# Performance work log

Measured on AMD Instinct MI355X. Metric: run time of the kernel, lower is better.

## Reference

```python
import jax, jax.numpy as jnp
import numpy as np

B, S, D = 2, 1024, 1024
H, HD = 16, 64          # n_heads, head_dim (H*HD == D)
E, FF = 8, 2816         # num_experts, moe hidden_dim
TOP_K = 2               # hard-coded torch.topk(scores, 2)
EPS = 1e-5


def rmsnorm(x, w):
    return x * jax.lax.rsqrt(jnp.mean(x * x, axis=-1, keepdims=True) + EPS) * w


def apply_rope(x, cos, sin):
    # x: [B,S,H,HD]; cos/sin: [S,HD//2] -> interleaved rotary (llama style)
    xr, xi = x[..., 0::2], x[..., 1::2]
    c = cos[None, :, None, :]
    s = sin[None, :, None, :]
    out_r = xr * c - xi * s
    out_i = xr * s + xi * c
    return jnp.stack([out_r, out_i], axis=-1).reshape(x.shape)


def setup_inputs() -> dict:
    key = jax.random.key(0)
    ks = jax.random.split(key, 10)
    sc = 0.02
    pos = jnp.arange(S, dtype=jnp.float32)
    inv = 1.0 / (10000.0 ** (jnp.arange(0, HD, 2, dtype=jnp.float32) / HD))
    ang = pos[:, None] * inv[None, :]                       # [S, HD//2]
    return {
        "x": jax.random.normal(ks[0], (B, S, D), jnp.float32),
        "freqs_cos": jnp.cos(ang),
        "freqs_sin": jnp.sin(ang),
        "attn_norm_w": jnp.ones((D,), jnp.float32),
        "wq": jax.random.normal(ks[1], (D, D), jnp.float32) * sc,
        "wk": jax.random.normal(ks[2], (D, D), jnp.float32) * sc,
        "wv": jax.random.normal(ks[3], (D, D), jnp.float32) * sc,
        "wo": jax.random.normal(ks[4], (D, D), jnp.float32) * sc,
        "ffn_norm_w": jnp.ones((D,), jnp.float32),
        "gate_w": jax.random.normal(ks[5], (E, D), jnp.float32) * sc,
        "w1": jax.random.normal(ks[6], (E, FF, D), jnp.float32) * sc,
        "w2": jax.random.normal(ks[7], (E, FF, D), jnp.float32) * sc,
        "w3": jax.random.normal(ks[8], (E, FF, D), jnp.float32) * sc,
    }


def reference(x, freqs_cos, freqs_sin, attn_norm_w, wq, wk, wv, wo,
              ffn_norm_w, gate_w, w1, w2, w3):
    b, s, d = x.shape

    # ---- pre-norm attention + residual ----
    xn = rmsnorm(x, attn_norm_w)
    q = (xn @ wq.T).reshape(b, s, H, HD)
    k = (xn @ wk.T).reshape(b, s, H, HD)
    v = (xn @ wv.T).reshape(b, s, H, HD)
    q = apply_rope(q, freqs_cos, freqs_sin)
    k = apply_rope(k, freqs_cos, freqs_sin)
    scores = jnp.einsum("bqhd,bkhd->bhqk", q, k) / jnp.sqrt(jnp.float32(HD))
    causal = jnp.tril(jnp.ones((s, s), bool))
    scores = jnp.where(causal[None, None], scores, jnp.finfo(scores.dtype).min)
    attn = jax.nn.softmax(scores, axis=-1)
    o = jnp.einsum("bhqk,bkhd->bqhd", attn, v).reshape(b, s, d) @ wo.T
    h = x + o

    # ---- top-2 MoE FFN (math identical to gather-per-token einsums) ----
    t = rmsnorm(h, ffn_norm_w).reshape(-1, d)               # [T, D]
    T = t.shape[0]
    gate = t @ gate_w.T                                     # [T, E]
    expert_weights, expert_idx = jax.lax.top_k(gate, TOP_K)
    expert_weights = jax.nn.softmax(expert_weights, axis=-1)  # [T, 2]

    x1 = jax.nn.silu(jnp.einsum("td,efd->tef", t, w1))      # [T, E, FF]
    x3 = jnp.einsum("td,efd->tef", t, w3)                   # [T, E, FF]
    ta = jnp.arange(T)[:, None]
    g = x1[ta, expert_idx] * x3[ta, expert_idx]             # [T, 2, FF]
    gw = g * expert_weights[..., None]                      # fold routing weights
    h_full = jnp.zeros((T, E, FF), t.dtype).at[ta, expert_idx].add(gw)
    moe = jnp.einsum("tef,efd->td", h_full, w2)             # [T, D]

    return h + moe.reshape(b, s, d)
```

## Files before the change

kernel.cpp:

```cpp
#include <hip/hip_runtime.h>

#define DI __device__ __forceinline__

typedef __attribute__((ext_vector_type(8))) short short8;
typedef __attribute__((ext_vector_type(4))) float f32x4;

#define DM   1024
#define TT   2048
#define SEQ  1024
#define NHD  16
#define HDD  64
#define NE   8
#define FF   2816

DI ushort f2bf(float f){
  union { float f; unsigned u; } c; c.f = f;
  unsigned u = c.u;
  u += 0x7fffu + ((u >> 16) & 1u);
  return (ushort)(u >> 16);
}
DI float bf2f(ushort b){
  union { unsigned u; float f; } c; c.u = ((unsigned)b) << 16;
  return c.f;
}
DI unsigned pk2(float a, float b){ return (unsigned)f2bf(a) | ((unsigned)f2bf(b) << 16); }
DI uint2 mku2(unsigned a, unsigned b){ uint2 r; r.x = a; r.y = b; return r; }

DI f32x4 MFMA(short8 a, short8 b, f32x4 c){
  return __builtin_amdgcn_mfma_f32_16x16x32_bf16(a, b, c, 0, 0, 0);
}

DI void gload16(const void* g, void* l){
  __builtin_amdgcn_global_load_lds(
      (const __attribute__((address_space(1))) unsigned*)g,
      (__attribute__((address_space(3))) unsigned*)l, 16, 0, 0);
}

#define LDSWZB(row, p) (((row) * 128) + ((((p) ^ ((row) & 7))) * 16))

__global__ __launch_bounds__(256) void k_pre(
    const float* __restrict__ x, const float* __restrict__ anw,
    ushort* __restrict__ xh, ushort* __restrict__ xl,
    const float* __restrict__ wq, const float* __restrict__ wk,
    const float* __restrict__ wv, const float* __restrict__ wo,
    ushort* __restrict__ wqh, ushort* __restrict__ wql,
    ushort* __restrict__ wkh, ushort* __restrict__ wkl,
    ushort* __restrict__ wvh, ushort* __restrict__ wvl,
    ushort* __restrict__ woh, ushort* __restrict__ wol)
{
  int bid = blockIdx.x, tid = threadIdx.x;
  if (bid >= 2048) {
    int q = bid - 2048;
    int y = q >> 10;
    const float* W = y == 0 ? wq : (y == 1 ? wk : (y == 2 ? wv : wo));
    ushort* H = y == 0 ? wqh : (y == 1 ? wkh : (y == 2 ? wvh : woh));
    ushort* L = y == 0 ? wql : (y == 1 ? wkl : (y == 2 ? wvl : wol));
    int i = (q & 1023) * 256 + tid;
    float4 v = ((const float4*)W)[i];
    ushort h0 = f2bf(v.x), h1 = f2bf(v.y), h2 = f2bf(v.z), h3 = f2bf(v.w);
    ((uint2*)H)[i] = mku2((unsigned)h0 | ((unsigned)h1 << 16),
                          (unsigned)h2 | ((unsigned)h3 << 16));
    ((uint2*)L)[i] = mku2(pk2(v.x - bf2f(h0), v.y - bf2f(h1)),
                          pk2(v.z - bf2f(h2), v.w - bf2f(h3)));
    return;
  }
  int row = bid;
  float4 v = ((const float4*)(x + (size_t)row * DM))[tid];
  float ss = v.x*v.x + v.y*v.y + v.z*v.z + v.w*v.w;
#pragma unroll
  for (int m = 32; m >= 1; m >>= 1) ss += __shfl_xor(ss, m);
  __shared__ float sh[4];
  if ((tid & 63) == 0) sh[tid >> 6] = ss;
  __syncthreads();
  ss = sh[0] + sh[1] + sh[2] + sh[3];
  float rstd = 1.0f / sqrtf(ss * (1.0f / DM) + 1e-5f);
  float4 wv2 = ((const float4*)anw)[tid];
  float o0 = v.x * rstd * wv2.x, o1 = v.y * rstd * wv2.y;
  float o2 = v.z * rstd * wv2.z, o3 = v.w * rstd * wv2.w;
  ushort h0 = f2bf(o0), h1 = f2bf(o1), h2 = f2bf(o2), h3 = f2bf(o3);
  ((uint2*)(xh + (size_t)row * DM))[tid] =
      mku2((unsigned)h0 | ((unsigned)h1 << 16), (unsigned)h2 | ((unsigned)h3 << 16));
  ((uint2*)(xl + (size_t)row * DM))[tid] =
      mku2(pk2(o0 - bf2f(h0), o1 - bf2f(h1)), pk2(o2 - bf2f(h2), o3 - bf2f(h3)));
}

__global__ __launch_bounds__(256) void k_cw13(const float* __restrict__ w1,
                                              const float* __restrict__ w3,
                                              ushort* __restrict__ w1b,
                                              ushort* __restrict__ w3b)
{
  const float* src = blockIdx.y ? w3 : w1;
  ushort* dst = blockIdx.y ? w3b : w1b;
  const size_t N4 = (size_t)NE * FF * DM / 4;
  for (size_t i = (size_t)blockIdx.x * 256 + threadIdx.x; i < N4;
       i += (size_t)gridDim.x * 256) {
    float4 v = ((const float4*)src)[i];
    ((uint2*)dst)[i] = mku2(pk2(v.x, v.y), pk2(v.z, v.w));
  }
}

__global__ __launch_bounds__(256, 3) void k_gemm_qkv(
    const ushort* __restrict__ xh, const ushort* __restrict__ xl,
    const ushort* __restrict__ wqh, const ushort* __restrict__ wql,
    const ushort* __restrict__ wkh, const ushort* __restrict__ wkl,
    const ushort* __restrict__ wvh, const ushort* __restrict__ wvl,
    const float* __restrict__ fc, const float* __restrict__ fs,
    ushort* __restrict__ qh, ushort* __restrict__ ql,
    ushort* __restrict__ kh, ushort* __restrict__ kl,
    ushort* __restrict__ vh, ushort* __restrict__ vl,
    const float* __restrict__ w2, ushort* __restrict__ w2t)
{
  __shared__ __align__(16) char lds[49152];
  int bid = blockIdx.x, tid = threadIdx.x;

  if (bid >= 768) {
    ushort* lt = (ushort*)lds;
    int pid = bid - 768;
    for (int tt = pid; tt < 16*44*8; tt += 512) {
      int dt = tt & 15, rest = tt >> 4;
      int ft = rest % 44, e = rest / 44;
#pragma unroll
      for (int i = 0; i < 4; i++) {
        int c = tid + i*256;
        int r = c >> 4, q = c & 15;
        float4 v = *(const float4*)(w2 + ((size_t)e*FF + ft*64 + r) * DM + dt*64 + q*4);
        lt[(q*4+0)*72 + r] = f2bf(v.x);
        lt[(q*4+1)*72 + r] = f2bf(v.y);
        lt[(q*4+2)*72 + r] = f2bf(v.z);
        lt[(q*4+3)*72 + r] = f2bf(v.w);
      }
      __syncthreads();
#pragma unroll
      for (int i = 0; i < 2; i++) {
        int c = tid + i*256;
        int d = c >> 3, fq = c & 7;
        *(uint4*)(w2t + ((size_t)e*DM + dt*64 + d) * FF + ft*64 + fq*8) =
            *(const uint4*)&lt[d*72 + fq*8];
      }
      __syncthreads();
    }
    return;
  }

  char* Ah = lds;          char* Al = lds + 16384;
  char* Bh = lds + 32768;  char* Bl = lds + 40960;
  int which = bid >> 8;
  int rest = bid & 255;
  int bnn = rest & 15, bm = rest >> 4;
  const ushort* WH = which == 0 ? wqh : (which == 1 ? wkh : wvh);
  const ushort* WL = which == 0 ? wql : (which == 1 ? wkl : wvl);
  int lane = tid & 63, w = tid >> 6;
  int r0 = lane >> 3, pp = lane & 7;
  size_t asrc[4]; int adst[4];
#pragma unroll
  for (int i = 0; i < 4; i++) {
    int c = w * 4 + i;
    int row = c * 8 + r0;
    asrc[i] = (size_t)(bm * 128 + row) * DM + (pp ^ r0) * 8;
    adst[i] = c * 1024;
  }
  size_t bsrc[2]; int bdst[2];
#pragma unroll
  for (int i = 0; i < 2; i++) {
    int c = 2 * w + i;
    int row = c * 8 + r0;
    bsrc[i] = (size_t)(bnn * 64 + row) * DM + (pp ^ r0) * 8;
    bdst[i] = c * 1024;
  }
  f32x4 acc[2][4] = {};
  for (int kb = 0; kb < DM; kb += 64) {
    __syncthreads();
#pragma unroll
    for (int i = 0; i < 4; i++) {
      gload16(xh + asrc[i] + kb, Ah + adst[i]);
      gload16(xl + asrc[i] + kb, Al + adst[i]);
    }
#pragma unroll
    for (int i = 0; i < 2; i++) {
      gload16(WH + bsrc[i] + kb, Bh + bdst[i]);
      gload16(WL + bsrc[i] + kb, Bl + bdst[i]);
    }
    __syncthreads();
#pragma unroll
    for (int kk = 0; kk < 2; kk++) {
      int j = kk * 4 + (lane >> 4);
      short8 ar[2], al[2];
#pragma unroll
      for (int mi = 0; mi < 2; mi++) {
        int row = w * 32 + mi * 16 + (lane & 15);
        ar[mi] = *(const short8*)(Ah + LDSWZB(row, j));
        al[mi] = *(const short8*)(Al + LDSWZB(row, j));
      }
#pragma unroll
      for (int ni = 0; ni < 4; ni++) {
        int n = ni * 16 + (lane & 15);
        short8 b_h = *(const short8*)(Bh + LDSWZB(n, j));
        short8 b_l = *(const short8*)(Bl + LDSWZB(n, j));
#pragma unroll
        for (int mi = 0; mi < 2; mi++) {
          acc[mi][ni] = MFMA(ar[mi], b_h, acc[mi][ni]);
          acc[mi][ni] = MFMA(al[mi], b_h, acc[mi][ni]);
          acc[mi][ni] = MFMA(ar[mi], b_l, acc[mi][ni]);
        }
      }
    }
  }
  ushort* OH = which == 0 ? qh : kh;
  ushort* OL = which == 0 ? ql : kl;
#pragma unroll
  for (int mi = 0; mi < 2; mi++)
#pragma unroll
    for (int ni = 0; ni < 4; ni++)
#pragma unroll
      for (int r = 0; r < 4; r++) {
        int rg = bm*128 + w*32 + mi*16 + (lane >> 4)*4 + r;
        int cg = bnn*64 + ni*16 + (lane & 15);
        float v = acc[mi][ni][r];
        int b = rg >> 10, s = rg & 1023, hh = cg >> 6, hd = cg & 63;
        if (which <= 1) {
          float p = __shfl_xor(v, 1);
          int pi = hd >> 1;
          float c = fc[s*32 + pi], sn = fs[s*32 + pi];
          float rr = (hd & 1) ? (p * sn + v * c) : (v * c - p * sn);
          size_t o = ((size_t)(b*NHD + hh) * SEQ + s) * HDD + hd;
          ushort hv = f2bf(rr);
          OH[o] = hv; OL[o] = f2bf(rr - bf2f(hv));
        } else {
          size_t o = ((size_t)((b*NHD + hh)*HDD + hd)) * SEQ + s;
          ushort hv = f2bf(v);
          vh[o] = hv; vl[o] = f2bf(v - bf2f(hv));
        }
      }
}

__global__ __launch_bounds__(256) void k_attn_prep(
    const ushort* __restrict__ qh_, const ushort* __restrict__ ql_,
    const ushort* __restrict__ kh_, const ushort* __restrict__ kl_,
    const ushort* __restrict__ vh_, const ushort* __restrict__ vl_,
    ushort* __restrict__ oh_, ushort* __restrict__ ol_,
    const float* __restrict__ w1, const float* __restrict__ w3,
    ushort* __restrict__ w1b, ushort* __restrict__ w3b)
{
  __shared__ __align__(16) char smem[49152];
  int bid = blockIdx.x, tid = threadIdx.x;

  if (bid >= 512) {
    int pid = bid - 512;
    const size_t N4 = (size_t)NE * FF * DM / 4;
    for (size_t i = (size_t)pid * 256 + tid; i < N4; i += (size_t)512 * 256) {
      float4 v = ((const float4*)w1)[i];
      ((uint2*)w1b)[i] = mku2(pk2(v.x, v.y), pk2(v.z, v.w));
      float4 u = ((const float4*)w3)[i];
      ((uint2*)w3b)[i] = mku2(pk2(u.x, u.y), pk2(u.z, u.w));
    }
    return;
  }

  char* Kh = smem;          char* Kl = smem + 8192;
  char* Vh = smem + 16384;  char* Vl = smem + 24576;
  ushort* Ph = (ushort*)(smem + 32768);
  ushort* Pl = (ushort*)(smem + 40960);
  int qt = bid & 15, bh = bid >> 4;
  int lane = tid & 63, w = tid >> 6;
  int r0 = lane >> 3, pp = lane & 7;
  short8 qfh[2], qfl[2];
  int qrow = qt*64 + w*16 + (lane & 15);
#pragma unroll
  for (int ks = 0; ks < 2; ks++) {
    size_t g = ((size_t)bh * SEQ + qrow) * HDD + ks*32 + (lane >> 4)*8;
    qfh[ks] = *(const short8*)(qh_ + g);
    qfl[ks] = *(const short8*)(ql_ + g);
  }
  size_t kbase[2], vbase[2];
#pragma unroll
  for (int i = 0; i < 2; i++) {
    int c = 2*w + i;
    kbase[i] = ((size_t)bh * SEQ + c*8 + r0) * 64 + (pp ^ r0) * 8;
    vbase[i] = ((size_t)bh * 64 + c*8 + r0) * SEQ + (pp ^ r0) * 8;
  }
  f32x4 oacc[4] = {};
  float mrun[4], lrun[4];
#pragma unroll
  for (int r = 0; r < 4; r++) { mrun[r] = -1e30f; lrun[r] = 0.0f; }

  for (int kt = 0; kt <= qt; kt++) {
    __syncthreads();
#pragma unroll
    for (int i = 0; i < 2; i++) {
      int c = 2*w + i;
      size_t ko = kbase[i] + (size_t)kt * 64 * 64;
      size_t vo = vbase[i] + (size_t)kt * 64;
      gload16(kh_ + ko, Kh + c*1024);
      gload16(kl_ + ko, Kl + c*1024);
      gload16(vh_ + vo, Vh + c*1024);
      gload16(vl_ + vo, Vl + c*1024);
    }
    __syncthreads();
    f32x4 sa[4] = {};
#pragma unroll
    for (int j2 = 0; j2 < 4; j2++) {
#pragma unroll
      for (int ks = 0; ks < 2; ks++) {
        int kr = j2*16 + (lane & 15);
        int j = ks*4 + (lane >> 4);
        short8 b_h = *(const short8*)(Kh + LDSWZB(kr, j));
        short8 b_l = *(const short8*)(Kl + LDSWZB(kr, j));
        sa[j2] = MFMA(qfh[ks], b_h, sa[j2]);
        sa[j2] = MFMA(qfl[ks], b_h, sa[j2]);
        sa[j2] = MFMA(qfh[ks], b_l, sa[j2]);
      }
    }
    float sv[4][4];
#pragma unroll
    for (int j2 = 0; j2 < 4; j2++)
#pragma unroll
      for (int r = 0; r < 4; r++) {
        float xx = sa[j2][r] * 0.125f;
        if (kt == qt) {
          int kv = j2*16 + (lane & 15), qi = w*16 + (lane >> 4)*4 + r;
          if (kv > qi) xx = -1e30f;
        }
        sv[j2][r] = xx;
      }
#pragma unroll
    for (int r = 0; r < 4; r++) {
      float mx = fmaxf(fmaxf(sv[0][r], sv[1][r]), fmaxf(sv[2][r], sv[3][r]));
#pragma unroll
      for (int m = 8; m >= 1; m >>= 1) mx = fmaxf(mx, __shfl_xor(mx, m));
      float mn = fmaxf(mrun[r], mx);
      float alp = __expf(mrun[r] - mn);
      mrun[r] = mn;
      float rs = 0.0f;
#pragma unroll
      for (int j2 = 0; j2 < 4; j2++) { float pv = __expf(sv[j2][r] - mn); sv[j2][r] = pv; rs += pv; }
#pragma unroll
      for (int m = 8; m >= 1; m >>= 1) rs += __shfl_xor(rs, m);
      lrun[r] = lrun[r] * alp + rs;
#pragma unroll
      for (int hf = 0; hf < 4; hf++) oacc[hf][r] *= alp;
    }
#pragma unroll
    for (int j2 = 0; j2 < 4; j2++)
#pragma unroll
      for (int r = 0; r < 4; r++) {
        int row = (lane >> 4)*4 + r, col = j2*16 + (lane & 15);
        int d = w*1024 + row*64 + (((col >> 3) ^ (row & 7)) * 8) + (col & 7);
        ushort hv = f2bf(sv[j2][r]);
        Ph[d] = hv; Pl[d] = f2bf(sv[j2][r] - bf2f(hv));
      }
#pragma unroll
    for (int hf = 0; hf < 4; hf++) {
#pragma unroll
      for (int ks = 0; ks < 2; ks++) {
        int prow = lane & 15;
        int j = ks*4 + (lane >> 4);
        int pg = (j ^ (prow & 7)) * 8;
        short8 pfh = *(const short8*)&Ph[w*1024 + prow*64 + pg];
        short8 pfl = *(const short8*)&Pl[w*1024 + prow*64 + pg];
        int vrow = hf*16 + (lane & 15);
        short8 vfh = *(const short8*)(Vh + LDSWZB(vrow, j));
        short8 vfl = *(const short8*)(Vl + LDSWZB(vrow, j));
        oacc[hf] = MFMA(pfh, vfh, oacc[hf]);
        oacc[hf] = MFMA(pfl, vfh, oacc[hf]);
        oacc[hf] = MFMA(pfh, vfl, oacc[hf]);
      }
    }
  }
  int b = bh >> 4, h = bh & 15;
#pragma unroll
  for (int r = 0; r < 4; r++) {
    float li = 1.0f / lrun[r];
    int srow = qt*64 + w*16 + (lane >> 4)*4 + r;
#pragma unroll
    for (int hf = 0; hf < 4; hf++) {
      float v = oacc[hf][r] * li;
      size_t o = ((size_t)(b*SEQ + srow)) * DM + h*HDD + hf*16 + (lane & 15);
      ushort hv = f2bf(v);
      oh_[o] = hv; ol_[o] = f2bf(v - bf2f(hv));
    }
  }
}

__global__ __launch_bounds__(256, 4) void k_gemm_wo(
    const ushort* __restrict__ oh, const ushort* __restrict__ ol,
    const ushort* __restrict__ woh, const ushort* __restrict__ wol,
    const float* __restrict__ x, float* __restrict__ hb)
{
  __shared__ __align__(16) char lds[32768];
  char* Ah = lds;          char* Al = lds + 8192;
  char* Bh = lds + 16384;  char* Bl = lds + 24576;
  int bnn = blockIdx.x, bm = blockIdx.y;
  int tid = threadIdx.x, lane = tid & 63, w = tid >> 6;
  int r0 = lane >> 3, pp = lane & 7;
  size_t asrc[2], bsrc[2]; int cdst[2];
#pragma unroll
  for (int i = 0; i < 2; i++) {
    int c = w * 2 + i;
    int row = c * 8 + r0;
    asrc[i] = (size_t)(bm * 64 + row) * DM + (pp ^ r0) * 8;
    bsrc[i] = (size_t)(bnn * 64 + row) * DM + (pp ^ r0) * 8;
    cdst[i] = c * 1024;
  }
  f32x4 acc[4] = {};
  for (int kb = 0; kb < DM; kb += 64) {
    __syncthreads();
#pragma unroll
    for (int i = 0; i < 2; i++) {
      gload16(oh + asrc[i] + kb, Ah + cdst[i]);
      gload16(ol + asrc[i] + kb, Al + cdst[i]);
      gload16(woh + bsrc[i] + kb, Bh + cdst[i]);
      gload16(wol + bsrc[i] + kb, Bl + cdst[i]);
    }
    __syncthreads();
#pragma unroll
    for (int kk = 0; kk < 2; kk++) {
      int j = kk * 4 + (lane >> 4);
      int row = w * 16 + (lane & 15);
      short8 ar = *(const short8*)(Ah + LDSWZB(row, j));
      short8 al = *(const short8*)(Al + LDSWZB(row, j));
#pragma unroll
      for (int ni = 0; ni < 4; ni++) {
        int n = ni * 16 + (lane & 15);
        short8 b_h = *(const short8*)(Bh + LDSWZB(n, j));
        short8 b_l = *(const short8*)(Bl + LDSWZB(n, j));
        acc[ni] = MFMA(ar, b_h, acc[ni]);
        acc[ni] = MFMA(al, b_h, acc[ni]);
        acc[ni] = MFMA(ar, b_l, acc[ni]);
      }
    }
  }
#pragma unroll
  for (int ni = 0; ni < 4; ni++)
#pragma unroll
    for (int r = 0; r < 4; r++) {
      int rg = bm*64 + w*16 + (lane >> 4)*4 + r;
      int cg = bnn*64 + ni*16 + (lane & 15);
      hb[(size_t)rg * DM + cg] = x[(size_t)rg * DM + cg] + acc[ni][r];
    }
}

__global__ __launch_bounds__(256) void k_gate(
    const float* __restrict__ hb, const float* __restrict__ fw, const float* __restrict__ gwt,
    ushort* __restrict__ tb, int* __restrict__ idx, float* __restrict__ ew,
    int* __restrict__ cnt, int* __restrict__ pos)
{
  int t = blockIdx.x, tid = threadIdx.x;
  float4 v = ((const float4*)(hb + (size_t)t * DM))[tid];
  float ss = v.x*v.x + v.y*v.y + v.z*v.z + v.w*v.w;
#pragma unroll
  for (int m = 32; m >= 1; m >>= 1) ss += __shfl_xor(ss, m);
  __shared__ float sh[4];
  if ((tid & 63) == 0) sh[tid >> 6] = ss;
  __syncthreads();
  ss = sh[0] + sh[1] + sh[2] + sh[3];
  float rstd = 1.0f / sqrtf(ss * (1.0f / DM) + 1e-5f);
  float4 wv = ((const float4*)fw)[tid];
  float tv0 = v.x*rstd*wv.x, tv1 = v.y*rstd*wv.y, tv2 = v.z*rstd*wv.z, tv3 = v.w*rstd*wv.w;
  ((uint2*)(tb + (size_t)t * DM))[tid] = mku2(pk2(tv0, tv1), pk2(tv2, tv3));
  float ge[8];
#pragma unroll
  for (int e = 0; e < 8; e++) {
    float4 gv = ((const float4*)(gwt + (size_t)e * DM))[tid];
    float s = tv0*gv.x + tv1*gv.y + tv2*gv.z + tv3*gv.w;
#pragma unroll
    for (int m = 32; m >= 1; m >>= 1) s += __shfl_xor(s, m);
    ge[e] = s;
  }
  __shared__ float gsh[4][8];
  if ((tid & 63) == 0) {
#pragma unroll
    for (int e = 0; e < 8; e++) gsh[tid >> 6][e] = ge[e];
  }
  __syncthreads();
  if (tid == 0) {
    float lg[8];
#pragma unroll
    for (int e = 0; e < 8; e++) lg[e] = gsh[0][e] + gsh[1][e] + gsh[2][e] + gsh[3][e];
    int i0 = 0;
    for (int e = 1; e < 8; e++) if (lg[e] > lg[i0]) i0 = e;
    int i1 = (i0 == 0) ? 1 : 0;
    for (int e = 0; e < 8; e++) if (e != i0 && lg[e] > lg[i1]) i1 = e;
    float ex = __expf(lg[i1] - lg[i0]);
    idx[2*t] = i0; idx[2*t+1] = i1;
    ew[2*t] = 1.0f / (1.0f + ex); ew[2*t+1] = ex / (1.0f + ex);
    pos[2*t]   = atomicAdd(&cnt[i0], 1);
    pos[2*t+1] = atomicAdd(&cnt[i1], 1);
  }
}

__global__ __launch_bounds__(256) void k_offscatter(
    const int* __restrict__ cnt, int* __restrict__ off, int* __restrict__ tmap,
    const int* __restrict__ idx, int* __restrict__ ent, int* __restrict__ pos)
{
  __shared__ int soff[8];
  int tid = threadIdx.x;
  if (tid == 0) {
    int a = 0, nt = 0;
    for (int e = 0; e < 8; e++) {
      off[e] = a; soff[e] = a; a += cnt[e];
      int m = (cnt[e] + 127) >> 7;
      for (int j = 0; j < m; j++) { tmap[1 + nt] = (e << 8) | j; nt++; }
    }
    tmap[0] = nt;
  }
  __syncthreads();
  for (int s = tid; s < 2*TT; s += 256) {
    int e = idx[s];
    int g = soff[e] + pos[s];
    ent[g] = s;
    pos[s] = g;
  }
}

__global__ __launch_bounds__(256, 4) void k_moe13(
    const ushort* __restrict__ tb, const ushort* __restrict__ w1b, const ushort* __restrict__ w3b,
    const int* __restrict__ ent, const float* __restrict__ ew,
    const int* __restrict__ cnt, const int* __restrict__ off, const int* __restrict__ tmap,
    ushort* __restrict__ gb)
{
  int y = blockIdx.y;
  if (y >= tmap[0]) return;
  int tm = tmap[1 + y];
  int e = tm >> 8, mt = tm & 255;
  int nt = blockIdx.x;
  int cn = cnt[e], oe = off[e];
  __shared__ __align__(16) char lds[32768];
  char* Ab = lds;
  char* B1 = lds + 16384;
  char* B3 = lds + 24576;
  int tid = threadIdx.x, lane = tid & 63, w = tid >> 6;
  int wr = w >> 1, wc = w & 1;
  int r0 = lane >> 3, pp = lane & 7;

  const ushort* abase = tb + (pp ^ r0) * 8;
  unsigned aoff[4];
#pragma unroll
  for (int i = 0; i < 4; i++) {
    int c = w * 4 + i;
    int r = c * 8 + r0;
    int g = oe + mt * 128 + r; if (g > 2*TT - 1) g = 2*TT - 1;
    aoff[i] = (unsigned)((ent[g] >> 1) * DM);
  }
  size_t bofs[2];
#pragma unroll
  for (int i = 0; i < 2; i++) {
    int c = 2 * w + i;
    bofs[i] = ((size_t)e * FF + nt * 64 + c * 8 + r0) * DM + (pp ^ r0) * 8;
  }

  f32x4 acc1[4][2] = {}, acc3[4][2] = {};

  for (int kb = 0; kb < DM; kb += 64) {
    __syncthreads();
#pragma unroll
    for (int i = 0; i < 4; i++)
      gload16(abase + aoff[i] + kb, Ab + (w * 4 + i) * 1024);
#pragma unroll
    for (int i = 0; i < 2; i++) {
      gload16(w1b + bofs[i] + kb, B1 + (2 * w + i) * 1024);
      gload16(w3b + bofs[i] + kb, B3 + (2 * w + i) * 1024);
    }
    __syncthreads();
#pragma unroll
    for (int kk = 0; kk < 2; kk++) {
      int j = kk * 4 + (lane >> 4);
      short8 af[4];
#pragma unroll
      for (int mi = 0; mi < 4; mi++) {
        int row = wr * 64 + mi * 16 + (lane & 15);
        af[mi] = *(const short8*)(Ab + LDSWZB(row, j));
      }
#pragma unroll
      for (int ni = 0; ni < 2; ni++) {
        int n = wc * 32 + ni * 16 + (lane & 15);
        short8 b1f = *(const short8*)(B1 + LDSWZB(n, j));
        short8 b3f = *(const short8*)(B3 + LDSWZB(n, j));
#pragma unroll
        for (int mi = 0; mi < 4; mi++) {
          acc1[mi][ni] = MFMA(af[mi], b1f, acc1[mi][ni]);
          acc3[mi][ni] = MFMA(af[mi], b3f, acc3[mi][ni]);
        }
      }
    }
  }
#pragma unroll
  for (int mi = 0; mi < 4; mi++)
#pragma unroll
    for (int ni = 0; ni < 2; ni++)
#pragma unroll
      for (int r = 0; r < 4; r++) {
        int grow = mt * 128 + wr * 64 + mi * 16 + (lane >> 4) * 4 + r;
        if (grow < cn) {
          int g = oe + grow;
          float gwv = ew[ent[g]];
          int f = nt * 64 + wc * 32 + ni * 16 + (lane & 15);
          float x1 = acc1[mi][ni][r], x3 = acc3[mi][ni][r];
          float sg = x1 / (1.0f + __expf(-x1));
          gb[(size_t)g * FF + f] = f2bf(sg * x3 * gwv);
        }
      }
}

__global__ __launch_bounds__(256, 4) void k_moe2(
    const ushort* __restrict__ gb, const ushort* __restrict__ w2t,
    const int* __restrict__ cnt, const int* __restrict__ off, const int* __restrict__ tmap,
    float* __restrict__ mr)
{
  int y = blockIdx.y;
  if (y >= tmap[0]) return;
  int tm = tmap[1 + y];
  int e = tm >> 8, mt = tm & 255;
  int nt = blockIdx.x;
  int cn = cnt[e], oe = off[e];
  __shared__ __align__(16) char lds[24576];
  char* Ab = lds; char* Bb = lds + 16384;
  int tid = threadIdx.x, lane = tid & 63, w = tid >> 6;
  int r0 = lane >> 3, pp = lane & 7;

  const ushort* abase = gb + (pp ^ r0) * 8;
  unsigned aoff[4];
#pragma unroll
  for (int i = 0; i < 4; i++) {
    int c = w * 4 + i;
    int r = c * 8 + r0;
    int g = oe + mt * 128 + r; if (g > 2*TT - 1) g = 2*TT - 1;
    aoff[i] = (unsigned)(g * FF);
  }
  size_t bofs[2];
#pragma unroll
  for (int i = 0; i < 2; i++) {
    int c = 2 * w + i;
    bofs[i] = ((size_t)e * DM + nt * 64 + c * 8 + r0) * FF + (pp ^ r0) * 8;
  }

  f32x4 a2[2][4] = {};
  for (int kb = 0; kb < FF; kb += 64) {
    __syncthreads();
#pragma unroll
    for (int i = 0; i < 4; i++)
      gload16(abase + aoff[i] + kb, Ab + (w * 4 + i) * 1024);
#pragma unroll
    for (int i = 0; i < 2; i++)
      gload16(w2t + bofs[i] + kb, Bb + (2 * w + i) * 1024);
    __syncthreads();
#pragma unroll
    for (int kk = 0; kk < 2; kk++) {
      int j = kk * 4 + (lane >> 4);
      short8 af[2], bf[4];
#pragma unroll
      for (int mi = 0; mi < 2; mi++) {
        int row = w * 32 + mi * 16 + (lane & 15);
        af[mi] = *(const short8*)(Ab + LDSWZB(row, j));
      }
#pragma unroll
      for (int ni = 0; ni < 4; ni++) {
        int n = ni * 16 + (lane & 15);
        bf[ni] = *(const short8*)(Bb + LDSWZB(n, j));
      }
#pragma unroll
      for (int ni = 0; ni < 4; ni++)
#pragma unroll
        for (int mi = 0; mi < 2; mi++)
          a2[mi][ni] = MFMA(af[mi], bf[ni], a2[mi][ni]);
    }
  }
#pragma unroll
  for (int mi = 0; mi < 2; mi++)
#pragma unroll
    for (int ni = 0; ni < 4; ni++)
#pragma unroll
      for (int r = 0; r < 4; r++) {
        int grow = mt * 128 + w * 32 + mi * 16 + (lane >> 4) * 4 + r;
        if (grow < cn) {
          int cg = nt * 64 + ni * 16 + (lane & 15);
          mr[(size_t)(oe + grow) * DM + cg] = a2[mi][ni][r];
        }
      }
}

__global__ __launch_bounds__(256) void k_final(
    const float* __restrict__ hb, const float* __restrict__ mr,
    const int* __restrict__ pos, float* __restrict__ out)
{
  int t = blockIdx.x, tid = threadIdx.x;
  int g0 = pos[2*t], g1 = pos[2*t+1];
  float4 a  = ((const float4*)(hb + (size_t)t * DM))[tid];
  float4 m0 = ((const float4*)(mr + (size_t)g0 * DM))[tid];
  float4 m1 = ((const float4*)(mr + (size_t)g1 * DM))[tid];
  float4 o;
  o.x = a.x + m0.x + m1.x; o.y = a.y + m0.y + m1.y;
  o.z = a.z + m0.z + m1.z; o.w = a.w + m0.w + m1.w;
  ((float4*)(out + (size_t)t * DM))[tid] = o;
}

extern "C" void kernel_launch(void* const* d_in, const int* in_sizes, int n_in,
                              void* d_out, int out_size, void* d_ws, size_t ws_size,
                              hipStream_t stream)
{
  const float* x   = (const float*)d_in[0];
  const float* fc  = (const float*)d_in[1];
  const float* fs  = (const float*)d_in[2];
  const float* anw = (const float*)d_in[3];
  const float* wq  = (const float*)d_in[4];
  const float* wk  = (const float*)d_in[5];
  const float* wv  = (const float*)d_in[6];
  const float* wo  = (const float*)d_in[7];
  const float* fnw = (const float*)d_in[8];
  const float* gwm = (const float*)d_in[9];
  const float* w1  = (const float*)d_in[10];
  const float* w2  = (const float*)d_in[11];
  const float* w3  = (const float*)d_in[12];
  float* out = (float*)d_out;

  char* p = (char*)d_ws;
  auto alloc = [&](size_t n) { char* r = p; p += (n + 255) & ~(size_t)255; return r; };
  ushort* xnh = (ushort*)alloc((size_t)TT*DM*2);
  ushort* xnl = (ushort*)alloc((size_t)TT*DM*2);
  char*   pad = alloc((size_t)8*1024*1024);
  ushort* qh  = (ushort*)alloc((size_t)TT*DM*2);
  ushort* ql  = (ushort*)alloc((size_t)TT*DM*2);
  ushort* kh  = (ushort*)alloc((size_t)TT*DM*2);
  ushort* kl  = (ushort*)alloc((size_t)TT*DM*2);
  ushort* vh  = (ushort*)alloc((size_t)TT*DM*2);
  ushort* vl  = (ushort*)alloc((size_t)TT*DM*2);
  ushort* oh  = (ushort*)alloc((size_t)TT*DM*2);
  ushort* ol  = (ushort*)alloc((size_t)TT*DM*2);
  float*  hb  = (float*) alloc((size_t)TT*DM*4);
  ushort* tb  = (ushort*)alloc((size_t)TT*DM*2);
  ushort* w2t = (ushort*)alloc((size_t)NE*FF*DM*2);
  ushort* gb  = (ushort*)alloc((size_t)2*TT*FF*2);
  float*  mr  = (float*) alloc((size_t)2*TT*DM*4);
  int*    idx = (int*)   alloc((size_t)2*TT*4);
  float*  ew  = (float*) alloc((size_t)2*TT*4);
  int*    ent = (int*)   alloc((size_t)2*TT*4);
  int*    pos = (int*)   alloc((size_t)2*TT*4);
  int*    cnt = (int*)   alloc(32);
  int*    off = (int*)   alloc(32);
  int*    tmap= (int*)   alloc(256);
  (void)pad;

  ushort* wsp = (ushort*)mr;
  const size_t WN = (size_t)DM * DM;
  ushort* wqh = wsp;        ushort* wql = wsp + WN;
  ushort* wkh = wsp + 2*WN; ushort* wkl = wsp + 3*WN;
  ushort* wvh = wsp + 4*WN; ushort* wvl = wsp + 5*WN;
  ushort* woh = wsp + 6*WN; ushort* wol = wsp + 7*WN;

  ushort* w3b = (ushort*)alloc((size_t)NE*FF*DM*2);
  ushort* w1b_fresh = (ushort*)alloc((size_t)NE*FF*DM*2);
  bool big = ((size_t)(p - (char*)d_ws) <= ws_size);
  ushort* w1b = big ? w1b_fresh : (ushort*)d_ws;

  hipMemsetAsync(cnt, 0, 32, stream);
  k_pre<<<6144, 256, 0, stream>>>(x, anw, xnh, xnl, wq, wk, wv, wo,
      wqh, wql, wkh, wkl, wvh, wvl, woh, wol);
  k_gemm_qkv<<<1280, 256, 0, stream>>>(xnh, xnl,
      wqh, wql, wkh, wkl, wvh, wvl, fc, fs, qh, ql, kh, kl, vh, vl, w2, w2t);
  if (big) {
    k_attn_prep<<<1024, 256, 0, stream>>>(qh, ql, kh, kl, vh, vl, oh, ol,
        w1, w3, w1b, w3b);
  } else {
    k_attn_prep<<<512, 256, 0, stream>>>(qh, ql, kh, kl, vh, vl, oh, ol,
        w1, w3, w1b, w3b);
  }
  k_gemm_wo<<<dim3(16, 32), 256, 0, stream>>>(oh, ol, woh, wol, x, hb);
  k_gate<<<TT, 256, 0, stream>>>(hb, fnw, gwm, tb, idx, ew, cnt, pos);
  k_offscatter<<<1, 256, 0, stream>>>(cnt, off, tmap, idx, ent, pos);
  if (!big) {
    k_cw13<<<dim3(2048, 2), 256, 0, stream>>>(w1, w3, w1b, w3b);
  }
  k_moe13<<<dim3(44, 48), 256, 0, stream>>>(tb, w1b, w3b, ent, ew, cnt, off, tmap, gb);
  k_moe2<<<dim3(16, 48), 256, 0, stream>>>(gb, w2t, cnt, off, tmap, mr);
  k_final<<<TT, 256, 0, stream>>>(hb, mr, pos, out);
  (void)in_sizes; (void)n_in; (void)out_size;
}
```

Measured before the change: 391.7 us.

## Enlarge QKV GEMM tiles to 128x128 and move w2 transpose into Wo kernel

The QKV projection GEMM now uses 128x128 output tiles with a 2x2 warp layout (64 KB LDS, launch bounds lowered to 2 blocks/CU), giving 384 blocks instead of 768 compute blocks. This raises arithmetic intensity per loaded tile. The w2 bf16 transpose work that was piggybacked on extra QKV blocks is moved into extra blocks of the Wo GEMM launch, which has a 1D grid of 1024. The aim is to cut QKV global traffic and rebalance the side work onto a kernel that leaves more of the GPU idle. The cost is lower occupancy and fewer blocks in QKV, which may underfill the GPU's CUs.

```diff
diff --git a/kernel.cpp b/kernel.cpp
--- a/kernel.cpp
+++ b/kernel.cpp
@@ -99,7 +99,7 @@
   }
 }
 
-__global__ __launch_bounds__(256, 3) void k_gemm_qkv(
+__global__ __launch_bounds__(256, 2) void k_gemm_qkv(
     const ushort* __restrict__ xh, const ushort* __restrict__ xl,
     const ushort* __restrict__ wqh, const ushort* __restrict__ wql,
     const ushort* __restrict__ wkh, const ushort* __restrict__ wkl,
@@ -107,97 +107,55 @@
     const float* __restrict__ fc, const float* __restrict__ fs,
     ushort* __restrict__ qh, ushort* __restrict__ ql,
     ushort* __restrict__ kh, ushort* __restrict__ kl,
-    ushort* __restrict__ vh, ushort* __restrict__ vl,
-    const float* __restrict__ w2, ushort* __restrict__ w2t)
-{
-  __shared__ __align__(16) char lds[49152];
+    ushort* __restrict__ vh, ushort* __restrict__ vl)
+{
+  __shared__ __align__(16) char lds[65536];
+  char* Ah = lds;          char* Al = lds + 16384;
+  char* Bh = lds + 32768;  char* Bl = lds + 49152;
   int bid = blockIdx.x, tid = threadIdx.x;
-
-  if (bid >= 768) {
-    ushort* lt = (ushort*)lds;
-    int pid = bid - 768;
-    for (int tt = pid; tt < 16*44*8; tt += 512) {
-      int dt = tt & 15, rest = tt >> 4;
-      int ft = rest % 44, e = rest / 44;
-#pragma unroll
-      for (int i = 0; i < 4; i++) {
-        int c = tid + i*256;
-        int r = c >> 4, q = c & 15;
-        float4 v = *(const float4*)(w2 + ((size_t)e*FF + ft*64 + r) * DM + dt*64 + q*4);
-        lt[(q*4+0)*72 + r] = f2bf(v.x);
-        lt[(q*4+1)*72 + r] = f2bf(v.y);
-        lt[(q*4+2)*72 + r] = f2bf(v.z);
-        lt[(q*4+3)*72 + r] = f2bf(v.w);
-      }
-      __syncthreads();
-#pragma unroll
-      for (int i = 0; i < 2; i++) {
-        int c = tid + i*256;
-        int d = c >> 3, fq = c & 7;
-        *(uint4*)(w2t + ((size_t)e*DM + dt*64 + d) * FF + ft*64 + fq*8) =
-            *(const uint4*)&lt[d*72 + fq*8];
-      }
-      __syncthreads();
-    }
-    return;
-  }
-
-  char* Ah = lds;          char* Al = lds + 16384;
-  char* Bh = lds + 32768;  char* Bl = lds + 40960;
-  int which = bid >> 8;
-  int rest = bid & 255;
-  int bnn = rest & 15, bm = rest >> 4;
+  int bn = bid % 24, bm = bid / 24;
+  int which = bn >> 3, bnn = bn & 7;
   const ushort* WH = which == 0 ? wqh : (which == 1 ? wkh : wvh);
   const ushort* WL = which == 0 ? wql : (which == 1 ? wkl : wvl);
-  int lane = tid & 63, w = tid >> 6;
+  int lane = tid & 63, w = tid >> 6, wr = w >> 1, wc = w & 1;
   int r0 = lane >> 3, pp = lane & 7;
-  size_t asrc[4]; int adst[4];
+  size_t asrc[4], bsrc[4]; int cdst[4];
 #pragma unroll
   for (int i = 0; i < 4; i++) {
     int c = w * 4 + i;
     int row = c * 8 + r0;
     asrc[i] = (size_t)(bm * 128 + row) * DM + (pp ^ r0) * 8;
-    adst[i] = c * 1024;
-  }
-  size_t bsrc[2]; int bdst[2];
-#pragma unroll
-  for (int i = 0; i < 2; i++) {
-    int c = 2 * w + i;
-    int row = c * 8 + r0;
-    bsrc[i] = (size_t)(bnn * 64 + row) * DM + (pp ^ r0) * 8;
-    bdst[i] = c * 1024;
-  }
-  f32x4 acc[2][4] = {};
+    bsrc[i] = (size_t)(bnn * 128 + row) * DM + (pp ^ r0) * 8;
+    cdst[i] = c * 1024;
+  }
+  f32x4 acc[4][4] = {};
   for (int kb = 0; kb < DM; kb += 64) {
     __syncthreads();
 #pragma unroll
     for (int i = 0; i < 4; i++) {
-      gload16(xh + asrc[i] + kb, Ah + adst[i]);
-      gload16(xl + asrc[i] + kb, Al + adst[i]);
-    }
-#pragma unroll
-    for (int i = 0; i < 2; i++) {
-      gload16(WH + bsrc[i] + kb, Bh + bdst[i]);
-      gload16(WL + bsrc[i] + kb, Bl + bdst[i]);
+      gload16(xh + asrc[i] + kb, Ah + cdst[i]);
+      gload16(xl + asrc[i] + kb, Al + cdst[i]);
+      gload16(WH + bsrc[i] + kb, Bh + cdst[i]);
+      gload16(WL + bsrc[i] + kb, Bl + cdst[i]);
     }
     __syncthreads();
 #pragma unroll
     for (int kk = 0; kk < 2; kk++) {
       int j = kk * 4 + (lane >> 4);
-      short8 ar[2], al[2];
-#pragma unroll
-      for (int mi = 0; mi < 2; mi++) {
-        int row = w * 32 + mi * 16 + (lane & 15);
+      short8 ar[4], al[4];
+#pragma unroll
+      for (int mi = 0; mi < 4; mi++) {
+        int row = wr * 64 + mi * 16 + (lane & 15);
         ar[mi] = *(const short8*)(Ah + LDSWZB(row, j));
         al[mi] = *(const short8*)(Al + LDSWZB(row, j));
       }
 #pragma unroll
       for (int ni = 0; ni < 4; ni++) {
-        int n = ni * 16 + (lane & 15);
+        int n = wc * 64 + ni * 16 + (lane & 15);
         short8 b_h = *(const short8*)(Bh + LDSWZB(n, j));
         short8 b_l = *(const short8*)(Bl + LDSWZB(n, j));
 #pragma unroll
-        for (int mi = 0; mi < 2; mi++) {
+        for (int mi = 0; mi < 4; mi++) {
           acc[mi][ni] = MFMA(ar[mi], b_h, acc[mi][ni]);
           acc[mi][ni] = MFMA(al[mi], b_h, acc[mi][ni]);
           acc[mi][ni] = MFMA(ar[mi], b_l, acc[mi][ni]);
@@ -208,13 +166,13 @@
   ushort* OH = which == 0 ? qh : kh;
   ushort* OL = which == 0 ? ql : kl;
 #pragma unroll
-  for (int mi = 0; mi < 2; mi++)
+  for (int mi = 0; mi < 4; mi++)
 #pragma unroll
     for (int ni = 0; ni < 4; ni++)
 #pragma unroll
       for (int r = 0; r < 4; r++) {
-        int rg = bm*128 + w*32 + mi*16 + (lane >> 4)*4 + r;
-        int cg = bnn*64 + ni*16 + (lane & 15);
+        int rg = bm*128 + wr*64 + mi*16 + (lane >> 4)*4 + r;
+        int cg = bnn*128 + wc*64 + ni*16 + (lane & 15);
         float v = acc[mi][ni][r];
         int b = rg >> 10, s = rg & 1023, hh = cg >> 6, hd = cg & 63;
         if (which <= 1) {
@@ -384,13 +342,45 @@
 __global__ __launch_bounds__(256, 4) void k_gemm_wo(
     const ushort* __restrict__ oh, const ushort* __restrict__ ol,
     const ushort* __restrict__ woh, const ushort* __restrict__ wol,
-    const float* __restrict__ x, float* __restrict__ hb)
+    const float* __restrict__ x, float* __restrict__ hb,
+    const float* __restrict__ w2, ushort* __restrict__ w2t)
 {
   __shared__ __align__(16) char lds[32768];
+  int bid = blockIdx.x, tid = threadIdx.x;
+
+  if (bid >= 512) {
+    ushort* lt = (ushort*)lds;
+    int pid = bid - 512;
+    for (int tt = pid; tt < 16*44*8; tt += 512) {
+      int dt = tt & 15, rest = tt >> 4;
+      int ft = rest % 44, e = rest / 44;
+#pragma unroll
+      for (int i = 0; i < 4; i++) {
+        int c = tid + i*256;
+        int r = c >> 4, q = c & 15;
+        float4 v = *(const float4*)(w2 + ((size_t)e*FF + ft*64 + r) * DM + dt*64 + q*4);
+        lt[(q*4+0)*72 + r] = f2bf(v.x);
+        lt[(q*4+1)*72 + r] = f2bf(v.y);
+        lt[(q*4+2)*72 + r] = f2bf(v.z);
+        lt[(q*4+3)*72 + r] = f2bf(v.w);
+      }
+      __syncthreads();
+#pragma unroll
+      for (int i = 0; i < 2; i++) {
+        int c = tid + i*256;
+        int d = c >> 3, fq = c & 7;
+        *(uint4*)(w2t + ((size_t)e*DM + dt*64 + d) * FF + ft*64 + fq*8) =
+            *(const uint4*)&lt[d*72 + fq*8];
+      }
+      __syncthreads();
+    }
+    return;
+  }
+
   char* Ah = lds;          char* Al = lds + 8192;
   char* Bh = lds + 16384;  char* Bl = lds + 24576;
-  int bnn = blockIdx.x, bm = blockIdx.y;
-  int tid = threadIdx.x, lane = tid & 63, w = tid >> 6;
+  int bnn = bid & 15, bm = bid >> 4;
+  int lane = tid & 63, w = tid >> 6;
   int r0 = lane >> 3, pp = lane & 7;
   size_t asrc[2], bsrc[2]; int cdst[2];
 #pragma unroll
@@ -754,8 +744,8 @@
   hipMemsetAsync(cnt, 0, 32, stream);
   k_pre<<<6144, 256, 0, stream>>>(x, anw, xnh, xnl, wq, wk, wv, wo,
       wqh, wql, wkh, wkl, wvh, wvl, woh, wol);
-  k_gemm_qkv<<<1280, 256, 0, stream>>>(xnh, xnl,
-      wqh, wql, wkh, wkl, wvh, wvl, fc, fs, qh, ql, kh, kl, vh, vl, w2, w2t);
+  k_gemm_qkv<<<384, 256, 0, stream>>>(xnh, xnl,
+      wqh, wql, wkh, wkl, wvh, wvl, fc, fs, qh, ql, kh, kl, vh, vl);
   if (big) {
     k_attn_prep<<<1024, 256, 0, stream>>>(qh, ql, kh, kl, vh, vl, oh, ol,
         w1, w3, w1b, w3b);
@@ -763,7 +753,7 @@
     k_attn_prep<<<512, 256, 0, stream>>>(qh, ql, kh, kl, vh, vl, oh, ol,
         w1, w3, w1b, w3b);
   }
-  k_gemm_wo<<<dim3(16, 32), 256, 0, stream>>>(oh, ol, woh, wol, x, hb);
+  k_gemm_wo<<<1024, 256, 0, stream>>>(oh, ol, woh, wol, x, hb, w2, w2t);
   k_gate<<<TT, 256, 0, stream>>>(hb, fnw, gwm, tb, idx, ew, cnt, pos);
   k_offscatter<<<1, 256, 0, stream>>>(cnt, off, tmap, idx, ent, pos);
   if (!big) {
```

New measurement: 388.9 us (median of 2 runs). Within noise of the previous version (-0.7%).
